# Kernel tuning notes

Hardware: AMD Instinct MI355X
Metric: run time of the kernel (lower is better)

The kernel has to match this reference:

```python
import jax, jax.numpy as jnp
import numpy as np

N, IN_C, D, H, M = 32768, 256, 64, 4, 4
P, S = 64, 512  # partitions x partition_size, P*S == N
SCALE = float(np.sqrt(D))


def setup_inputs() -> dict:
    key = jax.random.key(0)
    ks = jax.random.split(key, 12)
    lim_q = 1.0 / np.sqrt(IN_C)
    inp = {
        "x": jax.random.normal(ks[0], (N, IN_C), dtype=jnp.float32),
        "partition_indices": jnp.arange(N, dtype=jnp.int32).reshape(P, S),
        "boundary_scores": jax.random.uniform(ks[1], (N,), dtype=jnp.float32),
        "Wq_w": jax.random.uniform(ks[2], (H * D, IN_C), jnp.float32, -lim_q, lim_q),
        "Wq_b": jax.random.uniform(ks[3], (H * D,), jnp.float32, -lim_q, lim_q),
        "Wk_w": jax.random.uniform(ks[4], (H * D, IN_C), jnp.float32, -lim_q, lim_q),
        "Wk_b": jax.random.uniform(ks[5], (H * D,), jnp.float32, -lim_q, lim_q),
        "Wv_w": jax.random.uniform(ks[6], (H * D, IN_C), jnp.float32, -lim_q, lim_q),
        "Wv_b": jax.random.uniform(ks[7], (H * D,), jnp.float32, -lim_q, lim_q),
        "pool_seeds": jax.random.normal(ks[8], (M, H, D), dtype=jnp.float32) * 0.02,
        "alpha_logit": jnp.float32(0.0),
        "boundary_weight": jnp.float32(-1.0),
        "beta_logit": jnp.float32(0.0),
    }
    return inp


def reference(x, partition_indices, boundary_scores, Wq_w, Wq_b, Wk_w, Wk_b,
              Wv_w, Wv_b, pool_seeds, alpha_logit, boundary_weight, beta_logit):
    Q = (x @ Wq_w.T + Wq_b).reshape(N, H, D)
    K = (x @ Wk_w.T + Wk_b).reshape(N, H, D)
    V = (x @ Wv_w.T + Wv_b).reshape(N, H, D)

    # Gather per partition: [P, S, H, D]
    Qp = Q[partition_indices]
    Kp = K[partition_indices]
    Vp = V[partition_indices]

    # Local attention within each partition
    attn_local = jax.nn.softmax(
        jnp.einsum('pshd,pthd->phst', Qp, Kp) / SCALE, axis=-1)
    out_p = jnp.einsum('phst,pthd->pshd', attn_local, Vp)
    out_local = jnp.zeros((N, H, D), dtype=x.dtype).at[partition_indices.reshape(-1)].set(
        out_p.reshape(N, H, D))

    # Seed pooling per partition -> multi-resolution representatives
    pool_attn = jax.nn.softmax(
        jnp.einsum('mhd,pshd->pmhs', pool_seeds, Kp) / SCALE, axis=-1)
    reps_k = jnp.einsum('pmhs,pshd->pmhd', pool_attn, Kp).reshape(P * M, H, D)
    reps_v = jnp.einsum('pmhs,pshd->pmhd', pool_attn, Vp).reshape(P * M, H, D)

    x_local = out_local.mean(axis=1)

    # Global cross-attention over all representatives
    cross_attn = jax.nn.softmax(
        jnp.einsum('nhd,rhd->nhr', Q, reps_k) / SCALE, axis=-1)
    out_global = jnp.einsum('nhr,rhd->nhd', cross_attn, reps_v)
    x_global = out_global.mean(axis=1)

    x_self = V.mean(axis=1)

    alpha = jax.nn.sigmoid(alpha_logit + boundary_weight * boundary_scores)[:, None]
    beta = jax.nn.sigmoid(beta_logit) * 2.0
    return alpha * x_local + (1.0 - alpha) * x_global + beta * x_self
```

## Files before the change

### kernel.cpp

```cpp
#include <hip/hip_runtime.h>
#include <hip/hip_bf16.h>

#define N_TOK 32768
#define INC   256
#define HDIM  256
#define NH    4
#define DH    64
#define NP    64
#define SP    512
#define NM    4
#define NREPS 256
#define INV_SCALE 0.125f

typedef __attribute__((ext_vector_type(8))) __bf16 bf16x8;
typedef __attribute__((ext_vector_type(4))) float  f32x4;

static __device__ __forceinline__ ushort f2bf(float f) {
    __hip_bfloat16 h = __float2bfloat16(f);
    return *reinterpret_cast<ushort*>(&h);
}
static __device__ __forceinline__ float bf2f(ushort u) {
    return __uint_as_float(((uint)u) << 16);
}

#define GL_LDS16(g, l) __builtin_amdgcn_global_load_lds( \
    (const __attribute__((address_space(1))) unsigned int*)(g), \
    (__attribute__((address_space(3))) unsigned int*)(l), 16, 0, 0)

__global__ __launch_bounds__(256, 2) void qkv_mfma(
    const float* __restrict__ x,
    const float* __restrict__ Wq, const float* __restrict__ Wk,
    const float* __restrict__ Wv,
    const float* __restrict__ bq, const float* __restrict__ bk,
    const float* __restrict__ bv,
    ushort* __restrict__ Qb, ushort* __restrict__ Kb, ushort* __restrict__ Vb)
{
    const int bx = blockIdx.x;
    const int by = blockIdx.y;
    const int mat = by >> 1, nh = by & 1;
    const float* Wsel = (mat == 0) ? Wq : (mat == 1) ? Wk : Wv;
    const float* W = Wsel + (size_t)nh * 128 * 256;
    const float* bias = ((mat == 0) ? bq : (mat == 1) ? bk : bv) + nh * 128;
    ushort* outp = (mat == 0) ? Qb : (mat == 1) ? Kb : Vb;
    const float qscale = (mat == 0) ? INV_SCALE : 1.0f;
    const int rowBase = bx * 128;
    const int colBase = nh * 128;

    __shared__ ushort As[128 * 64];
    __shared__ ushort Bs[128 * 64];
    __shared__ ushort Cs[4][32][136];

    const int tid = threadIdx.x, wave = tid >> 6, lane = tid & 63;
    const int ln = lane & 15, lg = lane >> 4;

    f32x4 acc[2][8];
    #pragma unroll
    for (int mt = 0; mt < 2; ++mt)
        #pragma unroll
        for (int nt = 0; nt < 8; ++nt) acc[mt][nt] = (f32x4){0.f, 0.f, 0.f, 0.f};

    for (int k0 = 0; k0 < 256; k0 += 64) {
        __syncthreads();
        #pragma unroll
        for (int i = 0; i < 4; ++i) {
            int f = tid + 256 * i;
            int row = f >> 3, dc = f & 7;
            int pos = (dc ^ (row & 7)) << 3;
            {
                const float* src = &x[(size_t)(rowBase + row) * 256 + k0 + dc * 8];
                float4 a = *(const float4*)&src[0];
                float4 b = *(const float4*)&src[4];
                ushort u[8] = {f2bf(a.x), f2bf(a.y), f2bf(a.z), f2bf(a.w),
                               f2bf(b.x), f2bf(b.y), f2bf(b.z), f2bf(b.w)};
                *(int4*)&As[row * 64 + pos] = *(int4*)u;
            }
            {
                const float* src = &W[(size_t)row * 256 + k0 + dc * 8];
                float4 a = *(const float4*)&src[0];
                float4 b = *(const float4*)&src[4];
                ushort u[8] = {f2bf(a.x), f2bf(a.y), f2bf(a.z), f2bf(a.w),
                               f2bf(b.x), f2bf(b.y), f2bf(b.z), f2bf(b.w)};
                *(int4*)&Bs[row * 64 + pos] = *(int4*)u;
            }
        }
        __syncthreads();

        bf16x8 af[2][2], bfr[8][2];
        #pragma unroll
        for (int mt = 0; mt < 2; ++mt)
            #pragma unroll
            for (int kk = 0; kk < 2; ++kk) {
                int row = wave * 32 + mt * 16 + ln;
                int ch  = (kk * 4 + lg) ^ (row & 7);
                af[mt][kk] = *(const bf16x8*)&As[row * 64 + ch * 8];
            }
        #pragma unroll
        for (int nt = 0; nt < 8; ++nt)
            #pragma unroll
            for (int kk = 0; kk < 2; ++kk) {
                int n  = nt * 16 + ln;
                int ch = (kk * 4 + lg) ^ (n & 7);
                bfr[nt][kk] = *(const bf16x8*)&Bs[n * 64 + ch * 8];
            }
        #pragma unroll
        for (int mt = 0; mt < 2; ++mt)
            #pragma unroll
            for (int nt = 0; nt < 8; ++nt)
                #pragma unroll
                for (int kk = 0; kk < 2; ++kk)
                    acc[mt][nt] = __builtin_amdgcn_mfma_f32_16x16x32_bf16(
                        af[mt][kk], bfr[nt][kk], acc[mt][nt], 0, 0, 0);
    }

    float bvv[8];
    #pragma unroll
    for (int nt = 0; nt < 8; ++nt) bvv[nt] = bias[nt * 16 + ln];
    #pragma unroll
    for (int mt = 0; mt < 2; ++mt)
        #pragma unroll
        for (int nt = 0; nt < 8; ++nt)
            #pragma unroll
            for (int r = 0; r < 4; ++r)
                Cs[wave][mt * 16 + lg * 4 + r][nt * 16 + ln] =
                    f2bf((acc[mt][nt][r] + bvv[nt]) * qscale);
    __syncthreads();
    #pragma unroll
    for (int i = 0; i < 8; ++i) {
        int c = i * 64 + lane;
        int row = c >> 4, ch = c & 15;
        int4 v = *(const int4*)&Cs[wave][row][ch * 8];
        int outRow = rowBase + wave * 32 + row;
        *(int4*)&outp[(size_t)outRow * 256 + colBase + ch * 8] = v;
    }
}

__global__ __launch_bounds__(512) void pool_reps(
    const ushort* __restrict__ Kb, const ushort* __restrict__ Vb,
    const int* __restrict__ idx, const float* __restrict__ seeds,
    ushort* __restrict__ reps_k, ushort* __restrict__ reps_v)
{
    const int p = ((blockIdx.x & 7) << 3) | (blockIdx.x >> 3);
    const int h = blockIdx.y;
    const int tid = threadIdx.x;
    __shared__ float pexp[NM][SP];
    __shared__ float sums[NM];
    __shared__ float sred[NM][8];
    __shared__ float sd[NM][DH];
    __shared__ int   sidx[SP];

    if (tid < NM * DH) {
        int m = tid >> 6, d = tid & 63;
        sd[m][d] = seeds[(size_t)(m * NH + h) * DH + d];
    }
    sidx[tid] = idx[p * SP + tid];
    __syncthreads();

    const int n_s = sidx[tid];
    float kr[64];
    #pragma unroll
    for (int c = 0; c < 8; ++c) {
        int4 raw = *(const int4*)&Kb[(size_t)n_s * HDIM + h * DH + c * 8];
        const ushort* u = (const ushort*)&raw;
        #pragma unroll
        for (int j = 0; j < 8; ++j) kr[c * 8 + j] = bf2f(u[j]);
    }

    float e[NM];
    #pragma unroll
    for (int m = 0; m < NM; ++m) {
        float s = 0.f;
        #pragma unroll
        for (int d = 0; d < 64; ++d) s += kr[d] * sd[m][d];
        e[m] = __expf(s * INV_SCALE);
        pexp[m][tid] = e[m];
    }
    const int lane = tid & 63, w = tid >> 6;
    #pragma unroll
    for (int m = 0; m < NM; ++m) {
        float v = e[m];
        #pragma unroll
        for (int off = 32; off >= 1; off >>= 1) v += __shfl_xor(v, off);
        if (lane == 0) sred[m][w] = v;
    }
    __syncthreads();
    if (tid < NM) {
        float s = 0.f;
        #pragma unroll
        for (int i = 0; i < 8; ++i) s += sred[tid][i];
        sums[tid] = s;
    }
    __syncthreads();

    const int m = w >> 1, kv = w & 1, d = lane;
    const ushort* src = kv ? Vb : Kb;
    float acc = 0.f;
    #pragma unroll 8
    for (int s = 0; s < SP; ++s)
        acc += pexp[m][s] * bf2f(src[(size_t)sidx[s] * HDIM + h * DH + d]);
    ushort* dst = kv ? reps_v : reps_k;
    dst[(size_t)(p * NM + m) * HDIM + h * DH + d] = f2bf(acc / sums[m]);
}

template<int GATHER>
static __device__ __forceinline__ void attn_pass(
    const ushort* __restrict__ Kp, const ushort* __restrict__ Vp,
    const int* __restrict__ gidx, int nkeys, int hofs,
    ushort* Ks0, ushort* Ks1, ushort* Vt0, ushort* Vt1, ushort* Pw,
    const bf16x8 (&qf)[2][2], f32x4 (&oa)[4][2], float (&ssum)[2],
    int tid, int wave, int lane, int ln, int lg)
{
    const int kp = tid & 31, dc = tid >> 5;

    {
        #pragma unroll
        for (int i = 0; i < 2; ++i) {
            int r0  = wave * 16 + i * 8;
            int key = r0 + (lane >> 3);
            int cc  = (lane & 7) ^ (key & 7);
            int row = GATHER ? gidx[key] : key;
            GL_LDS16(&Kp[(size_t)row * HDIM + hofs + cc * 8], &Ks0[r0 * 64]);
        }
        int r0 = GATHER ? gidx[2 * kp] : 2 * kp;
        int r1 = GATHER ? gidx[2 * kp + 1] : 2 * kp + 1;
        int4 v0 = *(const int4*)&Vp[(size_t)r0 * HDIM + hofs + dc * 8];
        int4 v1 = *(const int4*)&Vp[(size_t)r1 * HDIM + hofs + dc * 8];
        const ushort* u0 = (const ushort*)&v0;
        const ushort* u1 = (const ushort*)&v1;
        #pragma unroll
        for (int j = 0; j < 8; ++j) {
            int d = dc * 8 + j;
            uint pk = (uint)u0[j] | ((uint)u1[j] << 16);
            *(uint*)&Vt0[d * 64 + (((kp >> 2) ^ (d & 7)) << 3) + (kp & 3) * 2] = pk;
        }
    }
    __syncthreads();

    const int nt = nkeys >> 6;
    for (int t = 0; t < nt; ++t) {
        ushort* KsC = (t & 1) ? Ks1 : Ks0;
        ushort* VtC = (t & 1) ? Vt1 : Vt0;
        ushort* KsN = (t & 1) ? Ks0 : Ks1;
        ushort* VtN = (t & 1) ? Vt0 : Vt1;
        const bool pfn = (t + 1 < nt);
        int4 v0, v1;
        if (pfn) {
            int kt0 = (t + 1) << 6;
            #pragma unroll
            for (int i = 0; i < 2; ++i) {
                int r0  = wave * 16 + i * 8;
                int key = r0 + (lane >> 3);
                int cc  = (lane & 7) ^ (key & 7);
                int row = GATHER ? gidx[kt0 + key] : (kt0 + key);
                GL_LDS16(&Kp[(size_t)row * HDIM + hofs + cc * 8], &KsN[r0 * 64]);
            }
            int r0 = GATHER ? gidx[kt0 + 2 * kp] : (kt0 + 2 * kp);
            int r1 = GATHER ? gidx[kt0 + 2 * kp + 1] : (kt0 + 2 * kp + 1);
            v0 = *(const int4*)&Vp[(size_t)r0 * HDIM + hofs + dc * 8];
            v1 = *(const int4*)&Vp[(size_t)r1 * HDIM + hofs + dc * 8];
        }

        #pragma unroll
        for (int ktile = 0; ktile < 4; ++ktile) {
            int kr = ktile * 16 + ln;
            bf16x8 ka0 = *(const bf16x8*)&KsC[kr * 64 + ((lg       ^ (kr & 7)) << 3)];
            bf16x8 ka1 = *(const bf16x8*)&KsC[kr * 64 + (((4 + lg) ^ (kr & 7)) << 3)];
            #pragma unroll
            for (int qt = 0; qt < 2; ++qt) {
                f32x4 s = (f32x4){0.f, 0.f, 0.f, 0.f};
                s = __builtin_amdgcn_mfma_f32_16x16x32_bf16(ka0, qf[qt][0], s, 0, 0, 0);
                s = __builtin_amdgcn_mfma_f32_16x16x32_bf16(ka1, qf[qt][1], s, 0, 0, 0);
                float p0 = __expf(s[0]);
                float p1 = __expf(s[1]);
                float p2 = __expf(s[2]);
                float p3 = __expf(s[3]);
                ssum[qt] += (p0 + p1) + (p2 + p3);
                uint lo = (uint)f2bf(p0) | ((uint)f2bf(p1) << 16);
                uint hi = (uint)f2bf(p2) | ((uint)f2bf(p3) << 16);
                int q  = qt * 16 + ln;
                int k0 = ktile * 16 + lg * 4;
                uint2 pk; pk.x = lo; pk.y = hi;
                *(uint2*)&Pw[q * 64 + (((k0 >> 3) ^ (q & 7)) << 3) + (k0 & 7)] = pk;
            }
        }

        bf16x8 pf[2][2];
        #pragma unroll
        for (int qt = 0; qt < 2; ++qt) {
            int q = qt * 16 + ln;
            #pragma unroll
            for (int kc = 0; kc < 2; ++kc) {
                int k0 = kc * 32 + lg * 8;
                pf[qt][kc] = *(const bf16x8*)&Pw[q * 64 + (((k0 >> 3) ^ (q & 7)) << 3)];
            }
        }
        #pragma unroll
        for (int dt = 0; dt < 4; ++dt) {
            int d = dt * 16 + ln;
            bf16x8 vf[2];
            #pragma unroll
            for (int kc = 0; kc < 2; ++kc) {
                int k0 = kc * 32 + lg * 8;
                vf[kc] = *(const bf16x8*)&VtC[d * 64 + (((k0 >> 3) ^ (d & 7)) << 3)];
            }
            #pragma unroll
            for (int qt = 0; qt < 2; ++qt)
                #pragma unroll
                for (int kc = 0; kc < 2; ++kc)
                    oa[dt][qt] = __builtin_amdgcn_mfma_f32_16x16x32_bf16(
                        vf[kc], pf[qt][kc], oa[dt][qt], 0, 0, 0);
        }

        if (pfn) {
            const ushort* u0 = (const ushort*)&v0;
            const ushort* u1 = (const ushort*)&v1;
            #pragma unroll
            for (int j = 0; j < 8; ++j) {
                int d = dc * 8 + j;
                uint pk = (uint)u0[j] | ((uint)u1[j] << 16);
                *(uint*)&VtN[d * 64 + (((kp >> 2) ^ (d & 7)) << 3) + (kp & 3) * 2] = pk;
            }
        }
        __syncthreads();
    }
}

__global__ __launch_bounds__(256, 3) void attn_fused(
    const ushort* __restrict__ Qb, const ushort* __restrict__ Kb,
    const ushort* __restrict__ Vb,
    const ushort* __restrict__ repk, const ushort* __restrict__ repv,
    const int* __restrict__ idx, const float* __restrict__ bscore,
    const float* __restrict__ alpha_logit, const float* __restrict__ bweight,
    const float* __restrict__ beta_logit,
    float* __restrict__ xc)
{
    const int work = ((blockIdx.x & 7) << 5) | (blockIdx.x >> 3);
    const int p = work >> 2, qc = work & 3;
    const int h = blockIdx.y;
    const int hofs = h * DH;
    const int tid  = threadIdx.x;
    const int wave = tid >> 6;
    const int lane = tid & 63;
    const int ln = lane & 15;
    const int lg = lane >> 4;

    __shared__ ushort Ks[2][64 * 64];
    __shared__ ushort Vt[2][64 * 64];
    __shared__ ushort Pb[4][32 * 64];
    ushort* Pw = Pb[wave];

    const int* gidx = idx + p * SP;

    bf16x8 qf[2][2];
    int tok[2];
    #pragma unroll
    for (int qt = 0; qt < 2; ++qt) {
        int qj = wave * 32 + qt * 16 + ln;
        int t  = gidx[qc * 128 + qj];
        tok[qt] = t;
        #pragma unroll
        for (int kc = 0; kc < 2; ++kc)
            qf[qt][kc] = *(const bf16x8*)&Qb[(size_t)t * HDIM + hofs + kc * 32 + lg * 8];
    }

    f32x4 oa_l[4][2], oa_g[4][2];
    float ssl[2] = {0.f, 0.f}, ssg[2] = {0.f, 0.f};
    #pragma unroll
    for (int dt = 0; dt < 4; ++dt)
        #pragma unroll
        for (int qt = 0; qt < 2; ++qt) {
            oa_l[dt][qt] = (f32x4){0.f, 0.f, 0.f, 0.f};
            oa_g[dt][qt] = (f32x4){0.f, 0.f, 0.f, 0.f};
        }

    attn_pass<1>(Kb, Vb, gidx, SP, hofs, Ks[0], Ks[1], Vt[0], Vt[1], Pw,
                 qf, oa_l, ssl, tid, wave, lane, ln, lg);
    attn_pass<0>(repk, repv, gidx, NREPS, hofs, Ks[0], Ks[1], Vt[0], Vt[1], Pw,
                 qf, oa_g, ssg, tid, wave, lane, ln, lg);

    const float al = alpha_logit[0], bw = bweight[0];
    const float beta25 = 0.25f * 2.f / (1.f + __expf(-beta_logit[0]));
    #pragma unroll
    for (int qt = 0; qt < 2; ++qt) {
        float sl = ssl[qt];
        sl += __shfl_xor(sl, 16);
        sl += __shfl_xor(sl, 32);
        float sg = ssg[qt];
        sg += __shfl_xor(sg, 16);
        sg += __shfl_xor(sg, 32);
        float a = 1.f / (1.f + __expf(-(al + bw * bscore[tok[qt]])));
        float wl = a * 0.25f / sl;
        float wg = (1.f - a) * 0.25f / sg;
        float* dst = &xc[((size_t)h * N_TOK + tok[qt]) * DH];
        const ushort* vsrc = &Vb[(size_t)tok[qt] * HDIM + hofs];
        #pragma unroll
        for (int dt = 0; dt < 4; ++dt) {
            uint2 vv = *(const uint2*)&vsrc[dt * 16 + lg * 4];
            float4 v;
            v.x = oa_l[dt][qt][0] * wl + oa_g[dt][qt][0] * wg + beta25 * bf2f((ushort)(vv.x & 0xffff));
            v.y = oa_l[dt][qt][1] * wl + oa_g[dt][qt][1] * wg + beta25 * bf2f((ushort)(vv.x >> 16));
            v.z = oa_l[dt][qt][2] * wl + oa_g[dt][qt][2] * wg + beta25 * bf2f((ushort)(vv.y & 0xffff));
            v.w = oa_l[dt][qt][3] * wl + oa_g[dt][qt][3] * wg + beta25 * bf2f((ushort)(vv.y >> 16));
            *(float4*)&dst[dt * 16 + lg * 4] = v;
        }
    }
}

__global__ __launch_bounds__(256) void combine(
    const float4* __restrict__ xc, float4* __restrict__ dout)
{
    const size_t PL = (size_t)N_TOK * DH / 4;
    const size_t i = (size_t)blockIdx.x * 256 + threadIdx.x;
    float4 a = xc[i], b = xc[i + PL], c = xc[i + 2 * PL], d = xc[i + 3 * PL];
    float4 o;
    o.x = a.x + b.x + c.x + d.x;
    o.y = a.y + b.y + c.y + d.y;
    o.z = a.z + b.z + c.z + d.z;
    o.w = a.w + b.w + c.w + d.w;
    dout[i] = o;
}

extern "C" void kernel_launch(void* const* d_in, const int* in_sizes, int n_in,
                              void* d_out, int out_size, void* d_ws, size_t ws_size,
                              hipStream_t stream)
{
    (void)in_sizes; (void)n_in; (void)ws_size; (void)out_size;
    const float* x      = (const float*)d_in[0];
    const int*   idx    = (const int*)d_in[1];
    const float* bscore = (const float*)d_in[2];
    const float* Wq = (const float*)d_in[3]; const float* bq = (const float*)d_in[4];
    const float* Wk = (const float*)d_in[5]; const float* bk = (const float*)d_in[6];
    const float* Wv = (const float*)d_in[7]; const float* bv = (const float*)d_in[8];
    const float* seeds = (const float*)d_in[9];
    const float* al = (const float*)d_in[10];
    const float* bw = (const float*)d_in[11];
    const float* bl = (const float*)d_in[12];
    float* out = (float*)d_out;

    const size_t NE = (size_t)N_TOK * HDIM;
    ushort* Qb    = (ushort*)d_ws;
    ushort* Kb    = Qb + NE;
    ushort* Vb    = Kb + NE;
    ushort* repkb = Vb + NE;
    ushort* repvb = repkb + (size_t)NREPS * HDIM;
    float*  xc    = (float*)(repvb + (size_t)NREPS * HDIM);

    qkv_mfma <<<dim3(256, 6), 256, 0, stream>>>(x, Wq, Wk, Wv, bq, bk, bv,
                                                Qb, Kb, Vb);
    pool_reps<<<dim3(NP, NH), 512, 0, stream>>>(Kb, Vb, idx, seeds, repkb, repvb);
    attn_fused<<<dim3(256, NH), 256, 0, stream>>>(Qb, Kb, Vb, repkb, repvb,
                                                  idx, bscore, al, bw, bl, xc);
    combine  <<<2048, 256, 0, stream>>>((const float4*)xc, (float4*)out);
}
```

Baseline: 208.8 us.

## Pre-convert inputs to bf16, restructure pool_reps, single-buffer V in attention

Adds a separate kernel that converts x and the three weight matrices to bf16 once, so the QKV GEMM can stage tiles with direct global-to-LDS loads instead of converting fp32 in every tile load. pool_reps now splits the sequence across waves and reuses each gathered K/V value for all four seeds, then reduces partial sums in shared memory. attn_fused single-buffers the transposed V tile, adding a barrier to free LDS, raises the occupancy hint to 4 blocks, and wraps the MFMA sections in s_setprio. The extra conversion kernel and the added barrier cost some time in exchange for these savings.

```diff
diff --git a/kernel.cpp b/kernel.cpp
--- a/kernel.cpp
+++ b/kernel.cpp
@@ -27,10 +27,35 @@
     (const __attribute__((address_space(1))) unsigned int*)(g), \
     (__attribute__((address_space(3))) unsigned int*)(l), 16, 0, 0)
 
-__global__ __launch_bounds__(256, 2) void qkv_mfma(
+__global__ __launch_bounds__(256) void conv_bf16(
     const float* __restrict__ x,
     const float* __restrict__ Wq, const float* __restrict__ Wk,
     const float* __restrict__ Wv,
+    ushort* __restrict__ xb, ushort* __restrict__ Wb)
+{
+    const int b = blockIdx.x, tid = threadIdx.x;
+    if (b < 4096) {
+        size_t base = (size_t)b * 2048 + tid * 8;
+        float4 a = *(const float4*)&x[base];
+        float4 c = *(const float4*)&x[base + 4];
+        ushort u[8] = {f2bf(a.x), f2bf(a.y), f2bf(a.z), f2bf(a.w),
+                       f2bf(c.x), f2bf(c.y), f2bf(c.z), f2bf(c.w)};
+        *(int4*)&xb[base] = *(int4*)u;
+    } else {
+        int wb = b - 4096;
+        const float* W = (wb < 32) ? Wq : (wb < 64) ? Wk : Wv;
+        int mat = wb >> 5;
+        size_t off = (size_t)(wb & 31) * 2048 + tid * 8;
+        float4 a = *(const float4*)&W[off];
+        float4 c = *(const float4*)&W[off + 4];
+        ushort u[8] = {f2bf(a.x), f2bf(a.y), f2bf(a.z), f2bf(a.w),
+                       f2bf(c.x), f2bf(c.y), f2bf(c.z), f2bf(c.w)};
+        *(int4*)&Wb[(size_t)mat * 65536 + off] = *(int4*)u;
+    }
+}
+
+__global__ __launch_bounds__(256, 2) void qkv_mfma(
+    const ushort* __restrict__ xb, const ushort* __restrict__ Wb,
     const float* __restrict__ bq, const float* __restrict__ bk,
     const float* __restrict__ bv,
     ushort* __restrict__ Qb, ushort* __restrict__ Kb, ushort* __restrict__ Vb)
@@ -38,8 +63,7 @@
     const int bx = blockIdx.x;
     const int by = blockIdx.y;
     const int mat = by >> 1, nh = by & 1;
-    const float* Wsel = (mat == 0) ? Wq : (mat == 1) ? Wk : Wv;
-    const float* W = Wsel + (size_t)nh * 128 * 256;
+    const ushort* W = Wb + (size_t)mat * 65536 + (size_t)nh * 128 * 256;
     const float* bias = ((mat == 0) ? bq : (mat == 1) ? bk : bv) + nh * 128;
     ushort* outp = (mat == 0) ? Qb : (mat == 1) ? Kb : Vb;
     const float qscale = (mat == 0) ? INV_SCALE : 1.0f;
@@ -63,25 +87,11 @@
         __syncthreads();
         #pragma unroll
         for (int i = 0; i < 4; ++i) {
-            int f = tid + 256 * i;
-            int row = f >> 3, dc = f & 7;
-            int pos = (dc ^ (row & 7)) << 3;
-            {
-                const float* src = &x[(size_t)(rowBase + row) * 256 + k0 + dc * 8];
-                float4 a = *(const float4*)&src[0];
-                float4 b = *(const float4*)&src[4];
-                ushort u[8] = {f2bf(a.x), f2bf(a.y), f2bf(a.z), f2bf(a.w),
-                               f2bf(b.x), f2bf(b.y), f2bf(b.z), f2bf(b.w)};
-                *(int4*)&As[row * 64 + pos] = *(int4*)u;
-            }
-            {
-                const float* src = &W[(size_t)row * 256 + k0 + dc * 8];
-                float4 a = *(const float4*)&src[0];
-                float4 b = *(const float4*)&src[4];
-                ushort u[8] = {f2bf(a.x), f2bf(a.y), f2bf(a.z), f2bf(a.w),
-                               f2bf(b.x), f2bf(b.y), f2bf(b.z), f2bf(b.w)};
-                *(int4*)&Bs[row * 64 + pos] = *(int4*)u;
-            }
+            int r0 = wave * 32 + i * 8;
+            int r  = r0 + (lane >> 3);
+            int cc = (lane & 7) ^ (r & 7);
+            GL_LDS16(&xb[(size_t)(rowBase + r) * 256 + k0 + cc * 8], &As[r0 * 64]);
+            GL_LDS16(&W[(size_t)r * 256 + k0 + cc * 8], &Bs[r0 * 64]);
         }
         __syncthreads();
 
@@ -147,6 +157,7 @@
     __shared__ float sred[NM][8];
     __shared__ float sd[NM][DH];
     __shared__ int   sidx[SP];
+    __shared__ float psum[2][NM][4][DH];
 
     if (tid < NM * DH) {
         int m = tid >> 6, d = tid & 63;
@@ -191,21 +202,40 @@
     }
     __syncthreads();
 
-    const int m = w >> 1, kv = w & 1, d = lane;
-    const ushort* src = kv ? Vb : Kb;
-    float acc = 0.f;
-    #pragma unroll 8
-    for (int s = 0; s < SP; ++s)
-        acc += pexp[m][s] * bf2f(src[(size_t)sidx[s] * HDIM + h * DH + d]);
-    ushort* dst = kv ? reps_v : reps_k;
-    dst[(size_t)(p * NM + m) * HDIM + h * DH + d] = f2bf(acc / sums[m]);
+    {
+        const int kv = w & 1, seg = w >> 1, d = lane;
+        const ushort* src = kv ? Vb : Kb;
+        float acc0 = 0.f, acc1 = 0.f, acc2 = 0.f, acc3 = 0.f;
+        const int s0 = seg * 128;
+        #pragma unroll 4
+        for (int s = s0; s < s0 + 128; ++s) {
+            float v = bf2f(src[(size_t)sidx[s] * HDIM + h * DH + d]);
+            acc0 += pexp[0][s] * v;
+            acc1 += pexp[1][s] * v;
+            acc2 += pexp[2][s] * v;
+            acc3 += pexp[3][s] * v;
+        }
+        psum[kv][0][seg][d] = acc0;
+        psum[kv][1][seg][d] = acc1;
+        psum[kv][2][seg][d] = acc2;
+        psum[kv][3][seg][d] = acc3;
+    }
+    __syncthreads();
+
+    {
+        const int kv = tid >> 8, m = (tid >> 6) & 3, d = tid & 63;
+        float r = (psum[kv][m][0][d] + psum[kv][m][1][d]) +
+                  (psum[kv][m][2][d] + psum[kv][m][3][d]);
+        ushort* dst = kv ? reps_v : reps_k;
+        dst[(size_t)(p * NM + m) * HDIM + h * DH + d] = f2bf(r / sums[m]);
+    }
 }
 
 template<int GATHER>
 static __device__ __forceinline__ void attn_pass(
     const ushort* __restrict__ Kp, const ushort* __restrict__ Vp,
     const int* __restrict__ gidx, int nkeys, int hofs,
-    ushort* Ks0, ushort* Ks1, ushort* Vt0, ushort* Vt1, ushort* Pw,
+    ushort* Ks0, ushort* Ks1, ushort* Vt, ushort* Pw,
     const bf16x8 (&qf)[2][2], f32x4 (&oa)[4][2], float (&ssum)[2],
     int tid, int wave, int lane, int ln, int lg)
 {
@@ -230,7 +260,7 @@
         for (int j = 0; j < 8; ++j) {
             int d = dc * 8 + j;
             uint pk = (uint)u0[j] | ((uint)u1[j] << 16);
-            *(uint*)&Vt0[d * 64 + (((kp >> 2) ^ (d & 7)) << 3) + (kp & 3) * 2] = pk;
+            *(uint*)&Vt[d * 64 + (((kp >> 2) ^ (d & 7)) << 3) + (kp & 3) * 2] = pk;
         }
     }
     __syncthreads();
@@ -238,9 +268,7 @@
     const int nt = nkeys >> 6;
     for (int t = 0; t < nt; ++t) {
         ushort* KsC = (t & 1) ? Ks1 : Ks0;
-        ushort* VtC = (t & 1) ? Vt1 : Vt0;
         ushort* KsN = (t & 1) ? Ks0 : Ks1;
-        ushort* VtN = (t & 1) ? Vt0 : Vt1;
         const bool pfn = (t + 1 < nt);
         int4 v0, v1;
         if (pfn) {
@@ -267,8 +295,10 @@
             #pragma unroll
             for (int qt = 0; qt < 2; ++qt) {
                 f32x4 s = (f32x4){0.f, 0.f, 0.f, 0.f};
+                __builtin_amdgcn_s_setprio(1);
                 s = __builtin_amdgcn_mfma_f32_16x16x32_bf16(ka0, qf[qt][0], s, 0, 0, 0);
                 s = __builtin_amdgcn_mfma_f32_16x16x32_bf16(ka1, qf[qt][1], s, 0, 0, 0);
+                __builtin_amdgcn_s_setprio(0);
                 float p0 = __expf(s[0]);
                 float p1 = __expf(s[1]);
                 float p2 = __expf(s[2]);
@@ -293,6 +323,7 @@
                 pf[qt][kc] = *(const bf16x8*)&Pw[q * 64 + (((k0 >> 3) ^ (q & 7)) << 3)];
             }
         }
+        __builtin_amdgcn_s_setprio(1);
         #pragma unroll
         for (int dt = 0; dt < 4; ++dt) {
             int d = dt * 16 + ln;
@@ -300,7 +331,7 @@
             #pragma unroll
             for (int kc = 0; kc < 2; ++kc) {
                 int k0 = kc * 32 + lg * 8;
-                vf[kc] = *(const bf16x8*)&VtC[d * 64 + (((k0 >> 3) ^ (d & 7)) << 3)];
+                vf[kc] = *(const bf16x8*)&Vt[d * 64 + (((k0 >> 3) ^ (d & 7)) << 3)];
             }
             #pragma unroll
             for (int qt = 0; qt < 2; ++qt)
@@ -309,7 +340,9 @@
                     oa[dt][qt] = __builtin_amdgcn_mfma_f32_16x16x32_bf16(
                         vf[kc], pf[qt][kc], oa[dt][qt], 0, 0, 0);
         }
-
+        __builtin_amdgcn_s_setprio(0);
+
+        __syncthreads();
         if (pfn) {
             const ushort* u0 = (const ushort*)&v0;
             const ushort* u1 = (const ushort*)&v1;
@@ -317,14 +350,14 @@
             for (int j = 0; j < 8; ++j) {
                 int d = dc * 8 + j;
                 uint pk = (uint)u0[j] | ((uint)u1[j] << 16);
-                *(uint*)&VtN[d * 64 + (((kp >> 2) ^ (d & 7)) << 3) + (kp & 3) * 2] = pk;
+                *(uint*)&Vt[d * 64 + (((kp >> 2) ^ (d & 7)) << 3) + (kp & 3) * 2] = pk;
             }
         }
         __syncthreads();
     }
 }
 
-__global__ __launch_bounds__(256, 3) void attn_fused(
+__global__ __launch_bounds__(256, 4) void attn_fused(
     const ushort* __restrict__ Qb, const ushort* __restrict__ Kb,
     const ushort* __restrict__ Vb,
     const ushort* __restrict__ repk, const ushort* __restrict__ repv,
@@ -344,7 +377,7 @@
     const int lg = lane >> 4;
 
     __shared__ ushort Ks[2][64 * 64];
-    __shared__ ushort Vt[2][64 * 64];
+    __shared__ ushort Vt[64 * 64];
     __shared__ ushort Pb[4][32 * 64];
     ushort* Pw = Pb[wave];
 
@@ -372,9 +405,9 @@
             oa_g[dt][qt] = (f32x4){0.f, 0.f, 0.f, 0.f};
         }
 
-    attn_pass<1>(Kb, Vb, gidx, SP, hofs, Ks[0], Ks[1], Vt[0], Vt[1], Pw,
+    attn_pass<1>(Kb, Vb, gidx, SP, hofs, Ks[0], Ks[1], Vt, Pw,
                  qf, oa_l, ssl, tid, wave, lane, ln, lg);
-    attn_pass<0>(repk, repv, gidx, NREPS, hofs, Ks[0], Ks[1], Vt[0], Vt[1], Pw,
+    attn_pass<0>(repk, repv, gidx, NREPS, hofs, Ks[0], Ks[1], Vt, Pw,
                  qf, oa_g, ssg, tid, wave, lane, ln, lg);
 
     const float al = alpha_logit[0], bw = bweight[0];
@@ -443,9 +476,11 @@
     ushort* repkb = Vb + NE;
     ushort* repvb = repkb + (size_t)NREPS * HDIM;
     float*  xc    = (float*)(repvb + (size_t)NREPS * HDIM);
-
-    qkv_mfma <<<dim3(256, 6), 256, 0, stream>>>(x, Wq, Wk, Wv, bq, bk, bv,
-                                                Qb, Kb, Vb);
+    ushort* xb    = (ushort*)xc;
+    ushort* Wb    = xb + NE;
+
+    conv_bf16<<<4192, 256, 0, stream>>>(x, Wq, Wk, Wv, xb, Wb);
+    qkv_mfma <<<dim3(256, 6), 256, 0, stream>>>(xb, Wb, bq, bk, bv, Qb, Kb, Vb);
     pool_reps<<<dim3(NP, NH), 512, 0, stream>>>(Kb, Vb, idx, seeds, repkb, repvb);
     attn_fused<<<dim3(256, NH), 256, 0, stream>>>(Qb, Kb, Vb, repkb, repvb,
                                                   idx, bscore, al, bw, bl, xc);
```

Result: faster. 196.8 us (-5.7%).
